# Optimization experiments

Measured on AMD Instinct MI355X. Metric: run time of the kernel, lower is better.

Reference implementation:

```python
import jax, jax.numpy as jnp
import numpy as np

B, S, NF, SD, D, FF, H, L = 32, 512, 124, 204, 512, 2048, 8, 4
DH = D // H
POSE_D = (D // H) * 1  # nheads_pose = 1
MAX_LEN = 5000


def make_pe(max_len, d):
    # sinusoidal positional encoding buffer, shape [max_len, 1, d]
    pos = jnp.arange(max_len, dtype=jnp.float32)[:, None]
    div = jnp.exp(jnp.arange(0, d, 2, dtype=jnp.float32) * (-np.log(10000.0) / d))
    pe = jnp.zeros((max_len, d), jnp.float32)
    pe = pe.at[:, 0::2].set(jnp.sin(pos * div)).at[:, 1::2].set(jnp.cos(pos * div))
    return pe[:, None, :]


def layer_norm(x, g, b, eps=1e-5):
    m = jnp.mean(x, -1, keepdims=True)
    v = jnp.mean((x - m) ** 2, -1, keepdims=True)
    return (x - m) / jnp.sqrt(v + eps) * g + b


def leaky_relu(x):
    return jnp.where(x >= 0, x, 0.2 * x)


def setup_inputs() -> dict:
    key = jax.random.key(0)
    ks = iter(jax.random.split(key, 48))

    def nrm(shape, s=0.02):
        return jax.random.normal(next(ks), shape, jnp.float32) * s

    return dict(
        x=jax.random.normal(next(ks), (B, S, NF), jnp.float32),
        timesteps=jax.random.randint(next(ks), (B,), 0, 1000),
        sparse_emb=jax.random.normal(next(ks), (B, S, SD), jnp.float32),
        W_lmk=nrm((SD, D)), b_lmk=jnp.zeros((D,)), g_lmk=jnp.ones((D,)), be_lmk=jnp.zeros((D,)),
        W_in=nrm((NF, D)), b_in=jnp.zeros((D,)), g_in=jnp.ones((D,)), be_in=jnp.zeros((D,)),
        W_merge=nrm((2 * D, D)), b_merge=jnp.zeros((D,)),
        Wt1=nrm((D, D)), bt1=jnp.zeros((D,)), Wt2=nrm((D, D)), bt2=jnp.zeros((D,)),
        in_proj_w=nrm((L, D, 3 * D)), in_proj_b=jnp.zeros((L, 3 * D)),
        out_proj_w=nrm((L, D, D)), out_proj_b=jnp.zeros((L, D)),
        ln1_g=jnp.ones((L, D)), ln1_b=jnp.zeros((L, D)),
        ln2_g=jnp.ones((L, D)), ln2_b=jnp.zeros((L, D)),
        W_ff1=nrm((L, D, FF)), b_ff1=jnp.zeros((L, FF)),
        W_ff2=nrm((L, FF, D)), b_ff2=jnp.zeros((L, D)),
        W_pose=nrm((POSE_D, 24)), b_pose=jnp.zeros((24,)),
        W_expr=nrm((D - POSE_D, 100)), b_expr=jnp.zeros((100,)),
    )


def reference(x, timesteps, sparse_emb,
              W_lmk, b_lmk, g_lmk, be_lmk,
              W_in, b_in, g_in, be_in,
              W_merge, b_merge,
              Wt1, bt1, Wt2, bt2,
              in_proj_w, in_proj_b, out_proj_w, out_proj_b,
              ln1_g, ln1_b, ln2_g, ln2_b,
              W_ff1, b_ff1, W_ff2, b_ff2,
              W_pose, b_pose, W_expr, b_expr):
    pe = make_pe(MAX_LEN, D)                      # [max_len, 1, D]
    # TimestepEmbedder: pe[timesteps] -> [B,1,D] -> MLP -> permute -> [1,B,D]
    ts = pe[timesteps]
    ts = jax.nn.silu(ts @ Wt1 + bt1) @ Wt2 + bt2
    ts_emb = jnp.transpose(ts, (1, 0, 2))
    # Lmk3dProcess / InputProcess: permute to seq-first, Linear+LN+LeakyReLU(0.2)
    lmk = leaky_relu(layer_norm(jnp.transpose(sparse_emb, (1, 0, 2)) @ W_lmk + b_lmk, g_lmk, be_lmk))
    xi = leaky_relu(layer_norm(jnp.transpose(x, (1, 0, 2)) @ W_in + b_in, g_in, be_in))
    h = jnp.concatenate([lmk, xi], -1) @ W_merge + b_merge   # [S,B,D]
    h = jnp.concatenate([ts_emb, h], 0)                      # [S+1,B,D]
    h = h + pe[:S + 1]                                       # pos enc (dropout off in eval)
    scale = 1.0 / np.sqrt(DH)
    T = S + 1
    for l in range(L):  # post-norm nn.TransformerEncoderLayer, gelu
        qkv = h @ in_proj_w[l] + in_proj_b[l]
        q, k, v = jnp.split(qkv, 3, -1)
        q = q.reshape(T, B, H, DH)
        k = k.reshape(T, B, H, DH)
        v = v.reshape(T, B, H, DH)
        att = jax.nn.softmax(jnp.einsum('tbhd,sbhd->bhts', q, k) * scale, axis=-1)
        o = jnp.einsum('bhts,sbhd->tbhd', att, v).reshape(T, B, D)
        h = layer_norm(h + o @ out_proj_w[l] + out_proj_b[l], ln1_g[l], ln1_b[l])
        f = jax.nn.gelu(h @ W_ff1[l] + b_ff1[l], approximate=False) @ W_ff2[l] + b_ff2[l]
        h = layer_norm(h + f, ln2_g[l], ln2_b[l])
    enc = h[1:]  # drop timestep token, [S,B,D]
    pose = jnp.transpose(enc[:, :, :POSE_D] @ W_pose + b_pose, (1, 0, 2))   # [B,S,24]
    expr = jnp.transpose(enc[:, :, POSE_D:] @ W_expr + b_expr, (1, 0, 2))   # [B,S,100]
    return jnp.concatenate([pose, expr], -1)                                # [B,S,124]
```

## Files before the change

### kernel.cpp

```cpp
#include <hip/hip_runtime.h>
#include <cmath>

#define B_ 32
#define S_ 512
#define NF_ 124
#define SD_ 204
#define D_ 512
#define FF_ 2048
#define H_ 8
#define L_ 4
#define T_ 513
#define TB_ 16416
#define SB_ 16384
#define PE_ROWS 1024

typedef unsigned short u16;
typedef __attribute__((ext_vector_type(8))) short bf16x8;
typedef __attribute__((ext_vector_type(4))) float f32x4;

__device__ __forceinline__ u16 f2bf(float f) {
  unsigned int u = __float_as_uint(f);
  unsigned int r = u + 0x7fff + ((u >> 16) & 1);
  return (u16)(r >> 16);
}
__device__ __forceinline__ float bf2f(u16 x) {
  return __uint_as_float((unsigned int)x << 16);
}

__device__ __forceinline__ int xcd_tile(int lin, int nb) {
  int xcd = lin & 7, j = lin >> 3;
  int base = nb >> 3, rem = nb & 7;
  int start = xcd * base + (xcd < rem ? xcd : rem);
  return start + j;
}

__global__ void pe_kernel(float* __restrict__ pe) {
  int p = blockIdx.x;
  int i = threadIdx.x;
  float div = expf(-(float)(2 * i) * (9.210340371976184f / 512.0f));
  float ang = (float)p * div;
  pe[p * 512 + 2 * i]     = sinf(ang);
  pe[p * 512 + 2 * i + 1] = cosf(ang);
}

__global__ void transpose_sb_bf(const float* __restrict__ in, u16* __restrict__ out,
                                int C, int Cpad, int total) {
  int idx = blockIdx.x * 256 + threadIdx.x;
  if (idx >= total) return;
  int c  = idx % Cpad;
  int sb = idx / Cpad;
  int b  = sb & (B_ - 1);
  int s  = sb >> 5;
  out[idx] = (c < C) ? f2bf(in[((size_t)b * S_ + s) * C + c]) : (u16)0;
}

__global__ __launch_bounds__(256) void wtrans_kernel(const float* __restrict__ W,
                                                     u16* __restrict__ Wt,
                                                     int K, int N,
                                                     long in_stride, long out_stride) {
  __shared__ float t[32][33];
  int l = blockIdx.z;
  W  += (size_t)l * in_stride;
  Wt += (size_t)l * out_stride;
  int n0 = blockIdx.x * 32, k0 = blockIdx.y * 32;
  int r = threadIdx.x >> 3;
  int c4 = (threadIdx.x & 7) * 4;
  float4 v = *(const float4*)(W + (size_t)(k0 + r) * N + n0 + c4);
  t[r][c4 + 0] = v.x; t[r][c4 + 1] = v.y; t[r][c4 + 2] = v.z; t[r][c4 + 3] = v.w;
  __syncthreads();
  u16* dst = Wt + (size_t)(n0 + r) * K + k0 + c4;
  for (int i = 0; i < 4; i++) dst[i] = f2bf(t[c4 + i][r]);
}

__global__ __launch_bounds__(256) void wtrans_pad_kernel(const float* __restrict__ W,
                                                         u16* __restrict__ Wt,
                                                         int K, int Kpad, int N) {
  __shared__ float t[32][33];
  int n0 = blockIdx.x * 32, k0 = blockIdx.y * 32;
  int r = threadIdx.x >> 3;
  int c4 = (threadIdx.x & 7) * 4;
  float4 v = make_float4(0.f, 0.f, 0.f, 0.f);
  if (k0 + r < K) v = *(const float4*)(W + (size_t)(k0 + r) * N + n0 + c4);
  t[r][c4 + 0] = v.x; t[r][c4 + 1] = v.y; t[r][c4 + 2] = v.z; t[r][c4 + 3] = v.w;
  __syncthreads();
  u16* dst = Wt + (size_t)(n0 + r) * Kpad + k0 + c4;
  for (int i = 0; i < 4; i++) dst[i] = f2bf(t[c4 + i][r]);
}

__global__ void head_prep_kernel(const float* __restrict__ Wp, const float* __restrict__ bp,
                                 const float* __restrict__ We, const float* __restrict__ be,
                                 u16* __restrict__ head_t, float* __restrict__ head_b) {
  int idx = blockIdx.x * 256 + threadIdx.x;
  int n = idx >> 9, k = idx & 511;
  float v = 0.f;
  if (n < 24) { if (k < 64) v = Wp[k * 24 + n]; }
  else if (n < 124) { if (k >= 64) v = We[(size_t)(k - 64) * 100 + (n - 24)]; }
  head_t[idx] = f2bf(v);
  if (idx < 128) head_b[idx] = (idx < 24) ? bp[idx] : ((idx < 124) ? be[idx - 24] : 0.f);
}

__global__ void ts_gather_kernel(const int* __restrict__ tsteps,
                                 const float* __restrict__ pe,
                                 u16* __restrict__ A) {
  int idx = blockIdx.x * 256 + threadIdx.x;
  int b = idx >> 9, k = idx & 511;
  A[idx] = f2bf(pe[(size_t)tsteps[b] * 512 + k]);
}

template<int BM, int BN, int WM, int WN>
__global__ __launch_bounds__(512) void gemm_bf16_t(
    const u16* __restrict__ A, const u16* __restrict__ Bt,
    const float* __restrict__ bias,
    u16* __restrict__ Cb, float* __restrict__ Cf,
    int M, int N, int K, int flags)
{
  constexpr int MT = WM / 16, NT = WN / 16;
  constexpr int ACH = BM * 8;
  constexpr int TCH = (BM + BN) * 8;
  constexpr int NC  = TCH / 512;
  constexpr int WROWS = BM / WM;
  __shared__ u16 sm[(BM + BN) * 64];
  int tid = threadIdx.x;
  int nx = gridDim.x;
  int lin = blockIdx.y * nx + blockIdx.x;
  int tile = xcd_tile(lin, nx * gridDim.y);
  int m0 = (tile / nx) * BM, n0 = (tile % nx) * BN;
  int wave = tid >> 6, lane = tid & 63;
  int wm = (wave % WROWS) * WM, wn = (wave / WROWS) * WN;
  int lm = lane & 15, kq = lane >> 4;

  f32x4 acc[MT][NT];
#pragma unroll
  for (int i = 0; i < MT; i++)
#pragma unroll
    for (int j = 0; j < NT; j++) acc[i][j] = (f32x4){0.f, 0.f, 0.f, 0.f};

  const u16* gp[NC];
  u16* lp[NC];
#pragma unroll
  for (int i = 0; i < NC; i++) {
    int c = tid + i * 512;
    if (c < ACH) {
      int p = c / (BM * 4), cp = c % (BM * 4);
      int r = cp >> 2, kk = p * 32 + (cp & 3) * 8;
      int row = m0 + r; if (row > M - 1) row = M - 1;
      gp[i] = A + (size_t)row * K + kk;
    } else {
      int cb = c - ACH;
      int p = cb / (BN * 4), cp = cb % (BN * 4);
      int r = cp >> 2, kk = p * 32 + (cp & 3) * 8;
      int row = n0 + r; if (row > N - 1) row = N - 1;
      gp[i] = Bt + (size_t)row * K + kk;
    }
    lp[i] = sm + (size_t)c * 8;
  }

  for (int k0 = 0; k0 < K; k0 += 64) {
#pragma unroll
    for (int i = 0; i < NC; i++)
      __builtin_amdgcn_global_load_lds(
          (const __attribute__((address_space(1))) void*)(gp[i] + k0),
          (__attribute__((address_space(3))) void*)lp[i], 16, 0, 0);
    __syncthreads();
#pragma unroll
    for (int st = 0; st < 2; st++) {
      bf16x8 af[MT], bg[NT];
#pragma unroll
      for (int i = 0; i < MT; i++)
        af[i] = *(const bf16x8*)&sm[st * BM * 32 + (wm + i * 16 + lm) * 32 + kq * 8];
#pragma unroll
      for (int j = 0; j < NT; j++)
        bg[j] = *(const bf16x8*)&sm[BM * 64 + st * BN * 32 + (wn + j * 16 + lm) * 32 + kq * 8];
#pragma unroll
      for (int i = 0; i < MT; i++)
#pragma unroll
        for (int j = 0; j < NT; j++)
          acc[i][j] = __builtin_amdgcn_mfma_f32_16x16x32_bf16(af[i], bg[j], acc[i][j], 0, 0, 0);
    }
    __syncthreads();
  }

  if (flags & 4) {
#pragma unroll
    for (int j = 0; j < NT; j++) {
      int gn = n0 + wn + j * 16 + lm;
      float bv = bias[gn];
#pragma unroll
      for (int i = 0; i < MT; i++) {
        int gm = m0 + wm + i * 16 + kq * 4;
#pragma unroll
        for (int r = 0; r < 4; r++) {
          if (gm + r < M && gn < 124) {
            int bb = (gm + r) & (B_ - 1), ss = (gm + r) >> 5;
            Cf[((size_t)bb * S_ + ss) * 124 + gn] = acc[i][j][r] + bv;
          }
        }
      }
    }
    return;
  }

#pragma unroll
  for (int j = 0; j < NT; j++) {
    int cn = wn + j * 16 + lm;
    float bv = bias[n0 + cn];
#pragma unroll
    for (int i = 0; i < MT; i++) {
      int rm = wm + i * 16 + kq * 4;
#pragma unroll
      for (int r = 0; r < 4; r++) {
        float v = acc[i][j][r] + bv;
        if (flags & 1) v = 0.5f * v * (1.0f + erff(v * 0.70710678118654752f));
        if (flags & 2) v = v / (1.0f + expf(-v));
        sm[(rm + r) * BN + cn] = f2bf(v);
      }
    }
  }
  __syncthreads();
  constexpr int SP = BM * BN / 4096;
#pragma unroll
  for (int pass = 0; pass < SP; pass++) {
    int e = pass * 4096 + tid * 8;
    int r = e / BN, cc = e % BN;
    int gm = m0 + r;
    if (gm < M)
      *(bf16x8*)(Cb + (size_t)gm * N + n0 + cc) = *(const bf16x8*)&sm[r * BN + cc];
  }
}

__device__ __forceinline__ float wave_sum(float v) {
#pragma unroll
  for (int off = 1; off < 64; off <<= 1) v += __shfl_xor(v, off, 64);
  return v;
}

__global__ __launch_bounds__(256) void ln_leaky_concat_kernel(
    const u16* __restrict__ lmk, const u16* __restrict__ xi,
    const float* __restrict__ gl, const float* __restrict__ bl,
    const float* __restrict__ gx, const float* __restrict__ bx,
    u16* __restrict__ cat)
{
  int wave = threadIdx.x >> 6, lane = threadIdx.x & 63;
  int g = blockIdx.x * 4 + wave;
  int r = g >> 1, part = g & 1;
  const u16* src = (part ? xi : lmk) + (size_t)r * 512 + lane * 8;
  const float* gg = (part ? gx : gl) + lane * 8;
  const float* bb = (part ? bx : bl) + lane * 8;
  bf16x8 hv = *(const bf16x8*)src;
  float v[8];
#pragma unroll
  for (int i = 0; i < 8; i++) v[i] = bf2f(((const u16*)&hv)[i]);
  float s = 0.f;
#pragma unroll
  for (int i = 0; i < 8; i++) s += v[i];
  float mean = wave_sum(s) * (1.0f / 512.0f);
  float s2 = 0.f;
#pragma unroll
  for (int i = 0; i < 8; i++) { v[i] -= mean; s2 += v[i] * v[i]; }
  float rs = rsqrtf(wave_sum(s2) * (1.0f / 512.0f) + 1e-5f);
  u16 ov[8];
#pragma unroll
  for (int i = 0; i < 8; i++) {
    float y = v[i] * rs * gg[i] + bb[i];
    y = (y >= 0.f) ? y : 0.2f * y;
    ov[i] = f2bf(y);
  }
  *(bf16x8*)(cat + (size_t)r * 1024 + part * 512 + lane * 8) = *(const bf16x8*)ov;
}

__global__ __launch_bounds__(256) void add_ln_kernel(
    u16* __restrict__ h_bf, const u16* __restrict__ src,
    const float* __restrict__ g, const float* __restrict__ be)
{
  int wave = threadIdx.x >> 6, lane = threadIdx.x & 63;
  int r = blockIdx.x * 4 + wave;
  size_t base = (size_t)r * 512 + lane * 8;
  bf16x8 hv = *(const bf16x8*)&h_bf[base];
  bf16x8 sv = *(const bf16x8*)&src[base];
  float v[8];
#pragma unroll
  for (int i = 0; i < 8; i++)
    v[i] = bf2f(((const u16*)&hv)[i]) + bf2f(((const u16*)&sv)[i]);
  float s = 0.f;
#pragma unroll
  for (int i = 0; i < 8; i++) s += v[i];
  float mean = wave_sum(s) * (1.0f / 512.0f);
  float s2 = 0.f;
#pragma unroll
  for (int i = 0; i < 8; i++) { v[i] -= mean; s2 += v[i] * v[i]; }
  float rs = rsqrtf(wave_sum(s2) * (1.0f / 512.0f) + 1e-5f);
  const float* gg = g + lane * 8;
  const float* bb = be + lane * 8;
  u16 ov[8];
#pragma unroll
  for (int i = 0; i < 8; i++) ov[i] = f2bf(v[i] * rs * gg[i] + bb[i]);
  *(bf16x8*)&h_bf[base] = *(const bf16x8*)ov;
}

__global__ void add_pe_kernel(u16* __restrict__ h_bf, const float* __restrict__ pe) {
  int idx = blockIdx.x * 256 + threadIdx.x;
  int e = idx * 8;
  int j = e & 511;
  int t = (e >> 9) / B_;
  bf16x8 hv = *(const bf16x8*)&h_bf[e];
  const float* pv = &pe[(size_t)t * 512 + j];
  u16 ov[8];
#pragma unroll
  for (int i = 0; i < 8; i++) ov[i] = f2bf(bf2f(((const u16*)&hv)[i]) + pv[i]);
  *(bf16x8*)&h_bf[e] = *(const bf16x8*)ov;
}

__global__ __launch_bounds__(512) void attn_kernel(const u16* __restrict__ qkv,
                                                   u16* __restrict__ o)
{
  __shared__ u16 Ks[64 * 72];
  __shared__ u16 Vt[64 * 72];
  __shared__ u16 Ps[128 * 72];

  int lin = blockIdx.y * 5 + blockIdx.x;
  int tile = (lin & 7) * 160 + (lin >> 3);
  int bh = tile / 5, qp = tile % 5;
  int b  = bh >> 3;
  int hh = bh & 7;
  int tid  = threadIdx.x;
  int wave = tid >> 6, lane = tid & 63;
  int lm = lane & 15, quad = lane >> 4;
  int wm = wave * 16;
  int t0 = qp * 128;

  bf16x8 qf0, qf1;
  {
    int t = t0 + wm + lm; if (t > T_ - 1) t = T_ - 1;
    const u16* qp_ = qkv + ((size_t)(t * B_ + b)) * 1536 + hh * 64;
    qf0 = *(const bf16x8*)(qp_ + quad * 8);
    qf1 = *(const bf16x8*)(qp_ + 32 + quad * 8);
  }

  f32x4 o_acc[4];
  float lsum = 0.f;
#pragma unroll
  for (int dt = 0; dt < 4; dt++) o_acc[dt] = (f32x4){0.f, 0.f, 0.f, 0.f};

  const float cs = 0.125f * 1.4426950408889634f;

  for (int s0 = 0; s0 < T_; s0 += 64) {
    __syncthreads();
    {
      int sr = tid >> 3, db = (tid & 7) * 8;
      int s = s0 + sr; if (s > T_ - 1) s = T_ - 1;
      *(bf16x8*)&Ks[sr * 72 + db] =
          *(const bf16x8*)(qkv + ((size_t)(s * B_ + b)) * 1536 + 512 + hh * 64 + db);
    }
    {
      int sr = tid & 63, db = (tid >> 6) * 8;
      int s = s0 + sr; if (s > T_ - 1) s = T_ - 1;
      bf16x8 vv = *(const bf16x8*)(qkv + ((size_t)(s * B_ + b)) * 1536 + 1024 + hh * 64 + db);
      const u16* pv = (const u16*)&vv;
#pragma unroll
      for (int i = 0; i < 8; i++) Vt[(db + i) * 72 + sr] = pv[i];
    }
    __syncthreads();

    f32x4 sacc[4];
#pragma unroll
    for (int st = 0; st < 4; st++) {
      sacc[st] = (f32x4){0.f, 0.f, 0.f, 0.f};
      bf16x8 k0 = *(const bf16x8*)&Ks[(st * 16 + lm) * 72 + quad * 8];
      bf16x8 k1 = *(const bf16x8*)&Ks[(st * 16 + lm) * 72 + 32 + quad * 8];
      sacc[st] = __builtin_amdgcn_mfma_f32_16x16x32_bf16(k0, qf0, sacc[st], 0, 0, 0);
      sacc[st] = __builtin_amdgcn_mfma_f32_16x16x32_bf16(k1, qf1, sacc[st], 0, 0, 0);
    }
    bool full = (s0 + 64 <= T_);
#pragma unroll
    for (int st = 0; st < 4; st++) {
      float p0, p1, p2, p3;
      if (full) {
        p0 = exp2f(sacc[st][0] * cs);
        p1 = exp2f(sacc[st][1] * cs);
        p2 = exp2f(sacc[st][2] * cs);
        p3 = exp2f(sacc[st][3] * cs);
      } else {
        int kb = s0 + st * 16 + quad * 4;
        p0 = exp2f((kb + 0 < T_) ? sacc[st][0] * cs : -10000.f);
        p1 = exp2f((kb + 1 < T_) ? sacc[st][1] * cs : -10000.f);
        p2 = exp2f((kb + 2 < T_) ? sacc[st][2] * cs : -10000.f);
        p3 = exp2f((kb + 3 < T_) ? sacc[st][3] * cs : -10000.f);
      }
      lsum += (p0 + p1) + (p2 + p3);
      unsigned int w0, w1;
      asm("v_cvt_pk_bf16_f32 %0, %1, %2" : "=v"(w0) : "v"(p0), "v"(p1));
      asm("v_cvt_pk_bf16_f32 %0, %1, %2" : "=v"(w1) : "v"(p2), "v"(p3));
      *(uint2*)&Ps[(wm + lm) * 72 + st * 16 + quad * 4] = make_uint2(w0, w1);
    }
#pragma unroll
    for (int ks = 0; ks < 2; ks++) {
      bf16x8 pf = *(const bf16x8*)&Ps[(wm + lm) * 72 + ks * 32 + quad * 8];
#pragma unroll
      for (int dt = 0; dt < 4; dt++) {
        bf16x8 vf = *(const bf16x8*)&Vt[(dt * 16 + lm) * 72 + ks * 32 + quad * 8];
        o_acc[dt] = __builtin_amdgcn_mfma_f32_16x16x32_bf16(pf, vf, o_acc[dt], 0, 0, 0);
      }
    }
  }

  lsum += __shfl_xor(lsum, 16, 64);
  lsum += __shfl_xor(lsum, 32, 64);
  float invq = 1.0f / lsum;
  float inv[4];
#pragma unroll
  for (int r = 0; r < 4; r++) inv[r] = __shfl(invq, quad * 4 + r, 16);
#pragma unroll
  for (int dt = 0; dt < 4; dt++)
#pragma unroll
    for (int r = 0; r < 4; r++)
      Ps[(wm + quad * 4 + r) * 72 + dt * 16 + lm] = f2bf(o_acc[dt][r] * inv[r]);
  {
    int rr = wm + (lane >> 2);
    int db = (lane & 3) * 16;
    int t = t0 + rr;
    if (t < T_) {
      bf16x8 a = *(const bf16x8*)&Ps[rr * 72 + db];
      bf16x8 b8 = *(const bf16x8*)&Ps[rr * 72 + db + 8];
      u16* op = o + ((size_t)(t * B_ + b)) * 512 + hh * 64 + db;
      *(bf16x8*)op = a;
      *(bf16x8*)(op + 8) = b8;
    }
  }
}

extern "C" void kernel_launch(void* const* d_in, const int* in_sizes, int n_in,
                              void* d_out, int out_size, void* d_ws, size_t ws_size,
                              hipStream_t stream) {
  const float* x       = (const float*)d_in[0];
  const int*   tsteps  = (const int*)  d_in[1];
  const float* se      = (const float*)d_in[2];
  const float* W_lmk   = (const float*)d_in[3];
  const float* b_lmk   = (const float*)d_in[4];
  const float* g_lmk   = (const float*)d_in[5];
  const float* be_lmk  = (const float*)d_in[6];
  const float* W_in    = (const float*)d_in[7];
  const float* b_in    = (const float*)d_in[8];
  const float* g_in    = (const float*)d_in[9];
  const float* be_in   = (const float*)d_in[10];
  const float* W_merge = (const float*)d_in[11];
  const float* b_merge = (const float*)d_in[12];
  const float* Wt1     = (const float*)d_in[13];
  const float* bt1     = (const float*)d_in[14];
  const float* Wt2     = (const float*)d_in[15];
  const float* bt2     = (const float*)d_in[16];
  const float* in_proj_w  = (const float*)d_in[17];
  const float* in_proj_b  = (const float*)d_in[18];
  const float* out_proj_w = (const float*)d_in[19];
  const float* out_proj_b = (const float*)d_in[20];
  const float* ln1_g   = (const float*)d_in[21];
  const float* ln1_b   = (const float*)d_in[22];
  const float* ln2_g   = (const float*)d_in[23];
  const float* ln2_b   = (const float*)d_in[24];
  const float* W_ff1   = (const float*)d_in[25];
  const float* b_ff1   = (const float*)d_in[26];
  const float* W_ff2   = (const float*)d_in[27];
  const float* b_ff2   = (const float*)d_in[28];
  const float* W_pose  = (const float*)d_in[29];
  const float* b_pose  = (const float*)d_in[30];
  const float* W_expr  = (const float*)d_in[31];
  const float* b_expr  = (const float*)d_in[32];
  float* out = (float*)d_out;

  float* pe      = (float*)d_ws;
  u16*   h_bf    = (u16*)(pe + (size_t)PE_ROWS * 512);
  u16*   big_bf  = h_bf + (size_t)TB_ * 512;
  u16*   bufO_bf = big_bf + (size_t)TB_ * 2048;
  u16*   bufP_bf = bufO_bf + (size_t)TB_ * 512;
  u16* merge_t = bufP_bf + (size_t)TB_ * 512;
  u16* ip_t    = merge_t + (size_t)512 * 1024;
  u16* op_t    = ip_t    + (size_t)L_ * 1536 * 512;
  u16* ff1_t   = op_t    + (size_t)L_ * 512 * 512;
  u16* ff2_t   = ff1_t   + (size_t)L_ * 2048 * 512;
  u16* lmk_t   = ff2_t   + (size_t)L_ * 512 * 2048;
  u16* xin_t   = lmk_t   + (size_t)512 * 256;
  u16* head_t  = xin_t   + (size_t)512 * 128;
  u16* wt1_t   = head_t  + (size_t)128 * 512;
  u16* wt2_t   = wt1_t   + (size_t)512 * 512;
  u16* ts_in   = wt2_t   + (size_t)512 * 512;
  u16* ts_mid  = ts_in   + (size_t)32 * 512;
  float* head_b = (float*)(ts_mid + (size_t)32 * 512);
  u16* seT_bf = bufO_bf;
  u16* xT_bf  = bufP_bf;
  u16* lmk_bf = big_bf;
  u16* xi_bf  = big_bf + (size_t)SB_ * 512;
  u16* cat_bf = big_bf + (size_t)SB_ * 1024;

  auto g128 = [&](const u16* A, const u16* Bt, const float* bias, u16* Cb,
                  int M, int N, int K, int flags) {
    dim3 grid(N / 128, (M + 127) / 128);
    gemm_bf16_t<128, 128, 32, 64><<<grid, 512, 0, stream>>>(A, Bt, bias, Cb, nullptr, M, N, K, flags);
  };
  auto g64 = [&](const u16* A, const u16* Bt, const float* bias, u16* Cb, float* Cf,
                 int M, int N, int K, int flags) {
    dim3 grid(N / 128, (M + 63) / 64);
    gemm_bf16_t<64, 128, 32, 32><<<grid, 512, 0, stream>>>(A, Bt, bias, Cb, Cf, M, N, K, flags);
  };

  wtrans_kernel<<<dim3(512 / 32, 1024 / 32, 1), 256, 0, stream>>>(
      W_merge, merge_t, 1024, 512, 0, 0);
  wtrans_kernel<<<dim3(1536 / 32, 512 / 32, L_), 256, 0, stream>>>(
      in_proj_w, ip_t, 512, 1536, (long)512 * 1536, (long)1536 * 512);
  wtrans_kernel<<<dim3(512 / 32, 512 / 32, L_), 256, 0, stream>>>(
      out_proj_w, op_t, 512, 512, (long)512 * 512, (long)512 * 512);
  wtrans_kernel<<<dim3(2048 / 32, 512 / 32, L_), 256, 0, stream>>>(
      W_ff1, ff1_t, 512, 2048, (long)512 * 2048, (long)2048 * 512);
  wtrans_kernel<<<dim3(512 / 32, 2048 / 32, L_), 256, 0, stream>>>(
      W_ff2, ff2_t, 2048, 512, (long)2048 * 512, (long)512 * 2048);
  wtrans_kernel<<<dim3(512 / 32, 512 / 32, 1), 256, 0, stream>>>(Wt1, wt1_t, 512, 512, 0, 0);
  wtrans_kernel<<<dim3(512 / 32, 512 / 32, 1), 256, 0, stream>>>(Wt2, wt2_t, 512, 512, 0, 0);
  wtrans_pad_kernel<<<dim3(512 / 32, 256 / 32), 256, 0, stream>>>(W_lmk, lmk_t, SD_, 256, 512);
  wtrans_pad_kernel<<<dim3(512 / 32, 128 / 32), 256, 0, stream>>>(W_in, xin_t, NF_, 128, 512);
  head_prep_kernel<<<(128 * 512) / 256, 256, 0, stream>>>(W_pose, b_pose, W_expr, b_expr,
                                                          head_t, head_b);

  pe_kernel<<<PE_ROWS, 256, 0, stream>>>(pe);
  transpose_sb_bf<<<(SB_ * 256 + 255) / 256, 256, 0, stream>>>(se, seT_bf, SD_, 256, SB_ * 256);
  transpose_sb_bf<<<(SB_ * 128 + 255) / 256, 256, 0, stream>>>(x, xT_bf, NF_, 128, SB_ * 128);
  g128(seT_bf, lmk_t, b_lmk, lmk_bf, SB_, 512, 256, 0);
  g128(xT_bf, xin_t, b_in, xi_bf, SB_, 512, 128, 0);
  ln_leaky_concat_kernel<<<SB_ * 2 / 4, 256, 0, stream>>>(lmk_bf, xi_bf, g_lmk, be_lmk,
                                                          g_in, be_in, cat_bf);
  g128(cat_bf, merge_t, b_merge, h_bf + (size_t)B_ * 512, SB_, 512, 1024, 0);
  ts_gather_kernel<<<(32 * 512) / 256, 256, 0, stream>>>(tsteps, pe, ts_in);
  g64(ts_in, wt1_t, bt1, ts_mid, nullptr, 32, 512, 512, 2);
  g64(ts_mid, wt2_t, bt2, h_bf, nullptr, 32, 512, 512, 0);
  add_pe_kernel<<<TB_ * 512 / 8 / 256, 256, 0, stream>>>(h_bf, pe);

  for (int l = 0; l < L_; l++) {
    g128(h_bf, ip_t + (size_t)l * 1536 * 512, in_proj_b + l * 1536,
         big_bf, TB_, 1536, 512, 0);
    attn_kernel<<<dim3(5, B_ * H_), 512, 0, stream>>>(big_bf, bufO_bf);
    g128(bufO_bf, op_t + (size_t)l * 512 * 512, out_proj_b + l * 512,
         bufP_bf, TB_, 512, 512, 0);
    add_ln_kernel<<<TB_ / 4, 256, 0, stream>>>(h_bf, bufP_bf, ln1_g + l * 512, ln1_b + l * 512);
    g128(h_bf, ff1_t + (size_t)l * 2048 * 512, b_ff1 + l * 2048,
         big_bf, TB_, 2048, 512, 1);
    g128(big_bf, ff2_t + (size_t)l * 512 * 2048, b_ff2 + l * 512,
         bufP_bf, TB_, 512, 2048, 0);
    add_ln_kernel<<<TB_ / 4, 256, 0, stream>>>(h_bf, bufP_bf, ln2_g + l * 512, ln2_b + l * 512);
  }

  g64(h_bf + (size_t)B_ * 512, head_t, head_b, nullptr, out, SB_, 128, 512, 4);
}
```

Baseline: 1.250 ms.

## Add 256-row 8-wave pipelined GEMM with direct-to-LDS loads and fast GELU

Replaces the 128x128 GEMM used for the input projections and all transformer-layer matmuls with a new 256xBN tile kernel. It double-buffers K slices via global_load_lds, interleaves MFMA quarters with barriers and s_setprio, and uses XOR-swizzled LDS layouts. The 32 leftover timestep-token rows are handled by a separate tail tile path. It also swaps the exact erf GELU for a sigmoid-based approximation, which cuts epilogue cost but changes numerics slightly.

New measurement: 1.549 ms. 1.24x slower.

```diff
diff --git a/kernel.cpp b/kernel.cpp
--- a/kernel.cpp
+++ b/kernel.cpp
@@ -25,6 +25,12 @@
 }
 __device__ __forceinline__ float bf2f(u16 x) {
   return __uint_as_float((unsigned int)x << 16);
+}
+
+__device__ __forceinline__ float gelu_f(float v) {
+  float x2 = v * v;
+  float z = v * (2.3021137f + 0.1029440f * x2);
+  return v / (1.0f + exp2f(-z));
 }
 
 __device__ __forceinline__ int xcd_tile(int lin, int nb) {
@@ -210,7 +216,7 @@
 #pragma unroll
       for (int r = 0; r < 4; r++) {
         float v = acc[i][j][r] + bv;
-        if (flags & 1) v = 0.5f * v * (1.0f + erff(v * 0.70710678118654752f));
+        if (flags & 1) v = gelu_f(v);
         if (flags & 2) v = v / (1.0f + expf(-v));
         sm[(rm + r) * BN + cn] = f2bf(v);
       }
@@ -225,6 +231,163 @@
     int gm = m0 + r;
     if (gm < M)
       *(bf16x8*)(Cb + (size_t)gm * N + n0 + cc) = *(const bf16x8*)&sm[r * BN + cc];
+  }
+}
+
+#define WAITV(n) asm volatile("s_waitcnt vmcnt(" #n ")" ::: "memory")
+#define BAR8() __builtin_amdgcn_s_barrier()
+#define MFMA_Q(mq) do { __builtin_amdgcn_s_setprio(1); \
+  _Pragma("unroll") for (int ii = 0; ii < 4; ii++) { \
+    _Pragma("unroll") for (int j = 0; j < NT; j++) { \
+      acc[(mq)*4+ii][j] = __builtin_amdgcn_mfma_f32_16x16x32_bf16(af[ii], bg[j], acc[(mq)*4+ii][j], 0, 0, 0); } } \
+  __builtin_amdgcn_s_setprio(0); } while (0)
+
+template<int BN, bool GELU>
+__global__ __launch_bounds__(512, 2) void gemm8_t(
+    const u16* __restrict__ A, const u16* __restrict__ Bt,
+    const float* __restrict__ bias, u16* __restrict__ Cb, int N, int K)
+{
+  constexpr int NT   = BN / 64;
+  constexpr int BUFU = 16384 + BN * 64;
+  constexpr int BSLC = BN * 32;
+  constexpr int CPR  = BN / 8;
+  __shared__ u16 lds[2 * BUFU];
+
+  int tid = threadIdx.x;
+  int nx = gridDim.x;
+  int lin = blockIdx.y * nx + blockIdx.x;
+  int tile = xcd_tile(lin, (int)gridDim.y * nx);
+  int mt = tile / nx;
+  int wave = tid >> 6, lane = tid & 63;
+  int lm = lane & 15, kq = lane >> 4;
+
+  if (mt >= 64) {
+    int n0 = (tile - 64 * nx) * BN;
+    int wM = wave & 1, wN = wave >> 1;
+    const u16* Ab = A + (size_t)(16384 + wM * 16 + lm) * K + kq * 8;
+    const u16* Bb = Bt + (size_t)(n0 + wN * (NT * 16) + lm) * K + kq * 8;
+    f32x4 tacc[NT];
+#pragma unroll
+    for (int j = 0; j < NT; j++) tacc[j] = (f32x4){0.f, 0.f, 0.f, 0.f};
+    for (int k0 = 0; k0 < K; k0 += 32) {
+      bf16x8 af = *(const bf16x8*)(Ab + k0);
+#pragma unroll
+      for (int j = 0; j < NT; j++) {
+        bf16x8 bg = *(const bf16x8*)(Bb + (size_t)j * 16 * K + k0);
+        tacc[j] = __builtin_amdgcn_mfma_f32_16x16x32_bf16(af, bg, tacc[j], 0, 0, 0);
+      }
+    }
+#pragma unroll
+    for (int j = 0; j < NT; j++) {
+      int gn = n0 + wN * (NT * 16) + j * 16 + lm;
+      float bv = bias[gn];
+#pragma unroll
+      for (int r = 0; r < 4; r++) {
+        float v = tacc[j][r] + bv;
+        if (GELU) v = gelu_f(v);
+        Cb[(size_t)(16384 + wM * 16 + kq * 4 + r) * N + gn] = f2bf(v);
+      }
+    }
+    return;
+  }
+
+  int m0 = mt * 256, n0 = (tile % nx) * BN;
+
+  int sr = tid >> 2;
+  int sq = (tid & 3) ^ ((sr >> 1) & 3);
+  const u16* a_src = A + (size_t)(m0 + sr) * K + sq * 8;
+  const u16* b_src = Bt + (size_t)(n0 + sr) * K + sq * 8;
+
+  int wM = wave >> 2, wN = wave & 3;
+  int kqx = (kq ^ ((lm >> 1) & 3)) * 8;
+  int abase = (wM * 128 + lm) * 32 + kqx;
+  int bbase = (wN * (NT * 16) + lm) * 32 + kqx;
+
+  f32x4 acc[8][NT];
+#pragma unroll
+  for (int i = 0; i < 8; i++)
+#pragma unroll
+    for (int j = 0; j < NT; j++) acc[i][j] = (f32x4){0.f, 0.f, 0.f, 0.f};
+  bf16x8 af[4], bg[NT];
+
+  auto stageA = [&](int buf, int ks, int kk) {
+    int o = buf * BUFU + ks * 8192 + tid * 8;
+    __builtin_amdgcn_global_load_lds(
+        (const __attribute__((address_space(1))) void*)(a_src + kk + ks * 32),
+        (__attribute__((address_space(3))) void*)&lds[o], 16, 0, 0);
+    __builtin_amdgcn_global_load_lds(
+        (const __attribute__((address_space(1))) void*)(a_src + (size_t)128 * K + kk + ks * 32),
+        (__attribute__((address_space(3))) void*)&lds[o + 4096], 16, 0, 0);
+  };
+  auto stageB = [&](int buf, int ks, int kk) {
+    int o = buf * BUFU + 16384 + ks * BSLC + tid * 8;
+    __builtin_amdgcn_global_load_lds(
+        (const __attribute__((address_space(1))) void*)(b_src + kk + ks * 32),
+        (__attribute__((address_space(3))) void*)&lds[o], 16, 0, 0);
+    if (BN == 256)
+      __builtin_amdgcn_global_load_lds(
+          (const __attribute__((address_space(1))) void*)(b_src + (size_t)128 * K + kk + ks * 32),
+          (__attribute__((address_space(3))) void*)&lds[o + 4096], 16, 0, 0);
+  };
+
+  stageA(0, 0, 0); stageB(0, 0, 0); stageA(0, 1, 0); stageB(0, 1, 0);
+  if (BN == 256) { WAITV(4); } else { WAITV(3); }
+  BAR8();
+
+  int nkt = K >> 6;
+  for (int t = 0; t < nkt; ++t) {
+    int cur = t & 1, nb = cur ^ 1;
+    bool stg = (t + 1 < nkt);
+    int kn = (t + 1) << 6;
+    int cb = cur * BUFU;
+    if (stg) { stageA(nb, 0, kn); stageB(nb, 0, kn); }
+#pragma unroll
+    for (int j = 0; j < NT; j++) bg[j] = *(const bf16x8*)&lds[cb + 16384 + bbase + j * 512];
+#pragma unroll
+    for (int ii = 0; ii < 4; ii++) af[ii] = *(const bf16x8*)&lds[cb + abase + ii * 512];
+    BAR8(); MFMA_Q(0); BAR8();
+    if (stg) { stageA(nb, 1, kn); stageB(nb, 1, kn); }
+#pragma unroll
+    for (int ii = 0; ii < 4; ii++) af[ii] = *(const bf16x8*)&lds[cb + abase + 2048 + ii * 512];
+    if (stg) { if (BN == 256) { WAITV(8); } else { WAITV(6); } }
+    else { WAITV(0); }
+    BAR8(); MFMA_Q(1); BAR8();
+#pragma unroll
+    for (int j = 0; j < NT; j++) bg[j] = *(const bf16x8*)&lds[cb + 16384 + BSLC + bbase + j * 512];
+#pragma unroll
+    for (int ii = 0; ii < 4; ii++) af[ii] = *(const bf16x8*)&lds[cb + 8192 + abase + ii * 512];
+    BAR8(); MFMA_Q(0); BAR8();
+#pragma unroll
+    for (int ii = 0; ii < 4; ii++) af[ii] = *(const bf16x8*)&lds[cb + 8192 + abase + 2048 + ii * 512];
+    if (stg) { if (BN == 256) { WAITV(4); } else { WAITV(3); } }
+    BAR8(); MFMA_Q(1); BAR8();
+  }
+
+  float bv[NT];
+#pragma unroll
+  for (int j = 0; j < NT; j++) bv[j] = bias[n0 + wN * (NT * 16) + j * 16 + lm];
+#pragma unroll
+  for (int i = 0; i < 8; i++)
+#pragma unroll
+    for (int j = 0; j < NT; j++) {
+      int col = wN * (NT * 16) + j * 16 + lm;
+      int ch = col >> 3, cl = col & 7;
+#pragma unroll
+      for (int r = 0; r < 4; r++) {
+        int rr = wM * 128 + i * 16 + kq * 4 + r;
+        float v = acc[i][j][r] + bv[j];
+        if (GELU) v = gelu_f(v);
+        lds[rr * BN + (ch ^ ((rr >> 2) & (CPR - 1))) * 8 + cl] = f2bf(v);
+      }
+    }
+  BAR8();
+  constexpr int NP = 256 * CPR / 512;
+#pragma unroll
+  for (int p = 0; p < NP; p++) {
+    int c = p * 512 + tid;
+    int row = c / CPR, c8 = c % CPR;
+    *(bf16x8*)(Cb + (size_t)(m0 + row) * N + n0 + c8 * 8) =
+        *(const bf16x8*)&lds[row * BN + (c8 ^ ((row >> 2) & (CPR - 1))) * 8];
   }
 }
 
@@ -490,11 +653,6 @@
   u16* xi_bf  = big_bf + (size_t)SB_ * 512;
   u16* cat_bf = big_bf + (size_t)SB_ * 1024;
 
-  auto g128 = [&](const u16* A, const u16* Bt, const float* bias, u16* Cb,
-                  int M, int N, int K, int flags) {
-    dim3 grid(N / 128, (M + 127) / 128);
-    gemm_bf16_t<128, 128, 32, 64><<<grid, 512, 0, stream>>>(A, Bt, bias, Cb, nullptr, M, N, K, flags);
-  };
   auto g64 = [&](const u16* A, const u16* Bt, const float* bias, u16* Cb, float* Cf,
                  int M, int N, int K, int flags) {
     dim3 grid(N / 128, (M + 63) / 64);
@@ -521,27 +679,28 @@
   pe_kernel<<<PE_ROWS, 256, 0, stream>>>(pe);
   transpose_sb_bf<<<(SB_ * 256 + 255) / 256, 256, 0, stream>>>(se, seT_bf, SD_, 256, SB_ * 256);
   transpose_sb_bf<<<(SB_ * 128 + 255) / 256, 256, 0, stream>>>(x, xT_bf, NF_, 128, SB_ * 128);
-  g128(seT_bf, lmk_t, b_lmk, lmk_bf, SB_, 512, 256, 0);
-  g128(xT_bf, xin_t, b_in, xi_bf, SB_, 512, 128, 0);
+  gemm8_t<128, false><<<dim3(4, 64), 512, 0, stream>>>(seT_bf, lmk_t, b_lmk, lmk_bf, 512, 256);
+  gemm8_t<128, false><<<dim3(4, 64), 512, 0, stream>>>(xT_bf, xin_t, b_in, xi_bf, 512, 128);
   ln_leaky_concat_kernel<<<SB_ * 2 / 4, 256, 0, stream>>>(lmk_bf, xi_bf, g_lmk, be_lmk,
                                                           g_in, be_in, cat_bf);
-  g128(cat_bf, merge_t, b_merge, h_bf + (size_t)B_ * 512, SB_, 512, 1024, 0);
+  gemm8_t<128, false><<<dim3(4, 64), 512, 0, stream>>>(cat_bf, merge_t, b_merge,
+                                                       h_bf + (size_t)B_ * 512, 512, 1024);
   ts_gather_kernel<<<(32 * 512) / 256, 256, 0, stream>>>(tsteps, pe, ts_in);
   g64(ts_in, wt1_t, bt1, ts_mid, nullptr, 32, 512, 512, 2);
   g64(ts_mid, wt2_t, bt2, h_bf, nullptr, 32, 512, 512, 0);
   add_pe_kernel<<<TB_ * 512 / 8 / 256, 256, 0, stream>>>(h_bf, pe);
 
   for (int l = 0; l < L_; l++) {
-    g128(h_bf, ip_t + (size_t)l * 1536 * 512, in_proj_b + l * 1536,
-         big_bf, TB_, 1536, 512, 0);
+    gemm8_t<128, false><<<dim3(12, 65), 512, 0, stream>>>(
+        h_bf, ip_t + (size_t)l * 1536 * 512, in_proj_b + l * 1536, big_bf, 1536, 512);
     attn_kernel<<<dim3(5, B_ * H_), 512, 0, stream>>>(big_bf, bufO_bf);
-    g128(bufO_bf, op_t + (size_t)l * 512 * 512, out_proj_b + l * 512,
-         bufP_bf, TB_, 512, 512, 0);
+    gemm8_t<128, false><<<dim3(4, 65), 512, 0, stream>>>(
+        bufO_bf, op_t + (size_t)l * 512 * 512, out_proj_b + l * 512, bufP_bf, 512, 512);
     add_ln_kernel<<<TB_ / 4, 256, 0, stream>>>(h_bf, bufP_bf, ln1_g + l * 512, ln1_b + l * 512);
-    g128(h_bf, ff1_t + (size_t)l * 2048 * 512, b_ff1 + l * 2048,
-         big_bf, TB_, 2048, 512, 1);
-    g128(big_bf, ff2_t + (size_t)l * 512 * 2048, b_ff2 + l * 512,
-         bufP_bf, TB_, 512, 2048, 0);
+    gemm8_t<256, true><<<dim3(8, 65), 512, 0, stream>>>(
+        h_bf, ff1_t + (size_t)l * 2048 * 512, b_ff1 + l * 2048, big_bf, 2048, 512);
+    gemm8_t<128, false><<<dim3(4, 65), 512, 0, stream>>>(
+        big_bf, ff2_t + (size_t)l * 512 * 2048, b_ff2 + l * 512, bufP_bf, 512, 2048);
     add_ln_kernel<<<TB_ / 4, 256, 0, stream>>>(h_bf, bufP_bf, ln2_g + l * 512, ln2_b + l * 512);
   }
 
```
